# Performance work log

Measured on AMD Instinct MI355X. Metric: run time of the kernel, lower is better.

Reference implementation:

```python
import jax, jax.numpy as jnp
import numpy as np

D_IN = 1024
D_OUT = 1024
NUM_HEADS = 16
HEAD_DIM = D_OUT // NUM_HEADS


def setup_inputs() -> dict:
    key = jax.random.key(0)
    ks = jax.random.split(key, 6)
    s = 0.02
    return {
        "x": jax.random.normal(ks[0], (4, 2048, D_IN), dtype=jnp.float32),
        "W_q": jax.random.normal(ks[1], (D_IN, D_OUT), dtype=jnp.float32) * s,
        "W_k": jax.random.normal(ks[2], (D_IN, D_OUT), dtype=jnp.float32) * s,
        "W_v": jax.random.normal(ks[3], (D_IN, D_OUT), dtype=jnp.float32) * s,
        "W_o": jax.random.normal(ks[4], (D_OUT, D_OUT), dtype=jnp.float32) * s,
        "b_o": jax.random.normal(ks[5], (D_OUT,), dtype=jnp.float32) * s,
    }


def reference(x, W_q, W_k, W_v, W_o, b_o):
    b, n, _ = x.shape
    # project and split heads: [b, h, n, d]
    q = (x @ W_q).reshape(b, n, NUM_HEADS, HEAD_DIM).transpose(0, 2, 1, 3)
    k = (x @ W_k).reshape(b, n, NUM_HEADS, HEAD_DIM).transpose(0, 2, 1, 3)
    v = (x @ W_v).reshape(b, n, NUM_HEADS, HEAD_DIM).transpose(0, 2, 1, 3)
    scores = jnp.einsum("bhqd,bhkd->bhqk", q, k)
    causal = jnp.tril(jnp.ones((n, n), dtype=bool))  # True = keep
    scores = jnp.where(causal, scores, -jnp.inf)
    attn = jax.nn.softmax(scores / np.sqrt(HEAD_DIM).astype(np.float32), axis=-1)
    ctx = jnp.einsum("bhqk,bhkd->bhqd", attn, v)
    ctx = ctx.transpose(0, 2, 1, 3).reshape(b, n, D_OUT)
    return ctx @ W_o + b_o
```

## Files before the change

### kernel.cpp

```cpp
#include <hip/hip_runtime.h>
#include <hip/hip_bf16.h>

#define NHEADS 16
#define HDIM 64
#define SEQ 2048
#define BATCH 4
#define DMODEL 1024
#define MTOT (BATCH * SEQ)

typedef short v8s __attribute__((ext_vector_type(8)));
typedef short v4s __attribute__((ext_vector_type(4)));
typedef float v4f __attribute__((ext_vector_type(4)));
typedef float v16f __attribute__((ext_vector_type(16)));
typedef unsigned int v4u __attribute__((ext_vector_type(4)));
typedef unsigned short u16;
typedef unsigned int u32;

__device__ __forceinline__ u16 f2bf(float f) {
    union { float f; unsigned u; } v; v.f = f;
    unsigned r = v.u + 0x7FFFu + ((v.u >> 16) & 1u);
    return (u16)(r >> 16);
}

__device__ __forceinline__ void g2l16(const u16* g, short* l) {
    __builtin_amdgcn_global_load_lds(
        (const __attribute__((address_space(1))) u32*)g,
        (__attribute__((address_space(3))) u32*)l, 16, 0, 0);
}

__device__ __forceinline__ unsigned pk_bf16(float a, float b) {
    unsigned r;
    asm("v_cvt_pk_bf16_f32 %0, %1, %2" : "=v"(r) : "v"(a), "v"(b));
    return r;
}
__device__ __forceinline__ void pl32swap(unsigned& x, unsigned& y) {
    asm("v_permlane32_swap_b32 %0, %1" : "+v"(x), "+v"(y));
}
__device__ __forceinline__ v8s build_pa(float a0, float a1, float a2, float a3,
                                        float b0, float b1, float b2, float b3) {
    unsigned X  = pk_bf16(a0, a1);
    unsigned X2 = pk_bf16(a2, a3);
    unsigned Y  = pk_bf16(b0, b1);
    unsigned Y2 = pk_bf16(b2, b3);
    pl32swap(X, Y);
    pl32swap(X2, Y2);
    v4u w; w[0] = X; w[1] = X2; w[2] = Y; w[3] = Y2;
    return __builtin_bit_cast(v8s, w);
}

__global__ __launch_bounds__(256)
void xcvt(const float* __restrict__ x, u16* __restrict__ xb)
{
    size_t i = ((size_t)blockIdx.x * 256 + threadIdx.x) * 8;
    v4f a = *(const v4f*)&x[i];
    v4f b = *(const v4f*)&x[i + 4];
    v8s p;
#pragma unroll
    for (int e = 0; e < 4; ++e) p[e] = (short)f2bf(a[e]);
#pragma unroll
    for (int e = 0; e < 4; ++e) p[4 + e] = (short)f2bf(b[e]);
    *(v8s*)&xb[i] = p;
}

__device__ __forceinline__ void transpose_body(
    const float* __restrict__ src, u16* __restrict__ dst, int k0, int n0)
{
    __shared__ __align__(8) short Ts[64 * 68];
    const int t = threadIdx.x;
    const int n4 = (t & 15) * 4, kl = t >> 4;
#pragma unroll
    for (int it = 0; it < 4; ++it) {
        int k = kl + 16 * it;
        v4f v = *(const v4f*)&src[(size_t)(k0 + k) * DMODEL + n0 + n4];
        v4s p;
#pragma unroll
        for (int e = 0; e < 4; ++e) p[e] = (short)f2bf(v[e]);
        *(v4s*)&Ts[k * 68 + n4] = p;
    }
    __syncthreads();
    const int nl = t >> 4, k4 = (t & 15) * 4;
#pragma unroll
    for (int it = 0; it < 4; ++it) {
        int n = nl + 16 * it;
        v4s o;
#pragma unroll
        for (int e = 0; e < 4; ++e) o[e] = Ts[(k4 + e) * 68 + n];
        *(v4s*)&dst[(size_t)(n0 + n) * DMODEL + k0 + k4] = o;
    }
}

__global__ __launch_bounds__(256)
void transpose_w(const float* __restrict__ src, u16* __restrict__ dst)
{
    transpose_body(src, dst, blockIdx.x * 64, blockIdx.y * 64);
}

__global__ __launch_bounds__(256)
void transpose_w4(const float* __restrict__ s0, const float* __restrict__ s1,
                  const float* __restrict__ s2, const float* __restrict__ s3,
                  u16* __restrict__ dst)
{
    const int z = blockIdx.z;
    const float* src = (z == 0) ? s0 : (z == 1) ? s1 : (z == 2) ? s2 : s3;
    transpose_body(src, dst + (size_t)z * DMODEL * DMODEL,
                   blockIdx.x * 64, blockIdx.y * 64);
}

#define QSCALE (0.125f * 1.44269504088896f)

__device__ __forceinline__ void qkv_epilogue(
    v4f (&acc)[4][4], int which, int n0, int m0, int wn, int wm,
    int l15, int quad, u16* Qb, u16* Kb, u16* Vt)
{
    if (which == 2) {
#pragma unroll
        for (int i = 0; i < 4; ++i)
#pragma unroll
            for (int j = 0; j < 4; ++j) {
                int col = n0 + wn + j * 16 + l15;
                int h = col >> 6, d = col & 63;
                int m = m0 + wm + i * 16 + quad * 4;
                int b = m >> 11, n = m & (SEQ - 1);
                v4s pv;
#pragma unroll
                for (int r = 0; r < 4; ++r) pv[r] = (short)f2bf(acc[i][j][r]);
                *(v4s*)&Vt[((size_t)(b * NHEADS + h) * HDIM + d) * SEQ + n] = pv;
            }
    } else {
        u16* Ob = (which == 0) ? Qb : Kb;
        const float scale = (which == 0) ? QSCALE : 1.0f;
#pragma unroll
        for (int i = 0; i < 4; ++i)
#pragma unroll
            for (int j = 0; j < 4; ++j) {
                int col = n0 + wn + j * 16 + l15;
                int h = col >> 6, d = col & 63;
#pragma unroll
                for (int r = 0; r < 4; ++r) {
                    int m = m0 + wm + i * 16 + quad * 4 + r;
                    int b = m >> 11, n = m & (SEQ - 1);
                    Ob[((size_t)(b * NHEADS + h) * SEQ + n) * HDIM + d] =
                        f2bf(acc[i][j][r] * scale);
                }
            }
    }
}

__global__ __launch_bounds__(256, 2)
void qkv_fast(const u16* __restrict__ xb, const u16* __restrict__ Wt,
              u16* __restrict__ Qb, u16* __restrict__ Kb, u16* __restrict__ Vt)
{
    __shared__ __align__(16) short As[128 * 64];
    __shared__ __align__(16) short Bs[128 * 64];

    const int which = blockIdx.z;
    const u16* W = Wt + (size_t)which * DMODEL * DMODEL;

    const int n0 = blockIdx.x * 128;
    const int m0 = blockIdx.y * 128;
    const int t = threadIdx.x;
    const int lane = t & 63;
    const int l15 = lane & 15;
    const int quad = lane >> 4;
    const int wave = t >> 6;
    const int wm = (wave >> 1) * 64;
    const int wn = (wave & 1) * 64;
    const int srow = t >> 3;
    const int sc8 = (t & 7) * 8;

    v4f acc[4][4];
#pragma unroll
    for (int i = 0; i < 4; ++i)
#pragma unroll
        for (int j = 0; j < 4; ++j) acc[i][j] = {0.f, 0.f, 0.f, 0.f};

    for (int k0 = 0; k0 < DMODEL; k0 += 64) {
        __syncthreads();
#pragma unroll
        for (int c = 0; c < 4; ++c) {
            g2l16(&xb[(size_t)(m0 + c * 32 + srow) * DMODEL + k0 + sc8],
                  &As[(c * 32 + srow) * 64 + sc8]);
            g2l16(&W[(size_t)(n0 + c * 32 + srow) * DMODEL + k0 + sc8],
                  &Bs[(c * 32 + srow) * 64 + sc8]);
        }
        __syncthreads();

#pragma unroll
        for (int kh = 0; kh < 2; ++kh) {
            v8s af[4], bf[4];
#pragma unroll
            for (int i = 0; i < 4; ++i)
                af[i] = *(const v8s*)
                    &As[(wm + i * 16 + l15) * 64 + kh * 32 + quad * 8];
#pragma unroll
            for (int j = 0; j < 4; ++j)
                bf[j] = *(const v8s*)
                    &Bs[(wn + j * 16 + l15) * 64 + kh * 32 + quad * 8];
#pragma unroll
            for (int i = 0; i < 4; ++i)
#pragma unroll
                for (int j = 0; j < 4; ++j)
                    acc[i][j] = __builtin_amdgcn_mfma_f32_16x16x32_bf16(
                        af[i], bf[j], acc[i][j], 0, 0, 0);
        }
    }
    qkv_epilogue(acc, which, n0, m0, wn, wm, l15, quad, Qb, Kb, Vt);
}

__global__ __launch_bounds__(256, 2)
void qkv_slow(const float* __restrict__ x, const u16* __restrict__ Wt,
              u16* __restrict__ Qb, u16* __restrict__ Kb, u16* __restrict__ Vt)
{
    __shared__ __align__(16) short As[128 * 32];
    __shared__ __align__(16) short Bs[128 * 32];

    const int which = blockIdx.z;
    const u16* W = Wt + (size_t)which * DMODEL * DMODEL;

    const int n0 = blockIdx.x * 128;
    const int m0 = blockIdx.y * 128;
    const int t = threadIdx.x;
    const int lane = t & 63;
    const int l15 = lane & 15;
    const int quad = lane >> 4;
    const int wave = t >> 6;
    const int wm = (wave >> 1) * 64;
    const int wn = (wave & 1) * 64;
    const int srow = t >> 2;
    const int sc8 = (t & 3) * 8;

    v4f acc[4][4];
#pragma unroll
    for (int i = 0; i < 4; ++i)
#pragma unroll
        for (int j = 0; j < 4; ++j) acc[i][j] = {0.f, 0.f, 0.f, 0.f};

    for (int k0 = 0; k0 < DMODEL; k0 += 32) {
        __syncthreads();
        g2l16(&W[(size_t)(n0 + srow) * DMODEL + k0 + sc8], &Bs[srow * 32 + sc8]);
        g2l16(&W[(size_t)(n0 + 64 + srow) * DMODEL + k0 + sc8],
              &Bs[(64 + srow) * 32 + sc8]);
#pragma unroll
        for (int it = 0; it < 2; ++it) {
            int row = srow + 64 * it;
            const float* xp = &x[(size_t)(m0 + row) * DMODEL + k0 + sc8];
            v4f x0 = *(const v4f*)xp;
            v4f x1 = *(const v4f*)(xp + 4);
            v8s av;
#pragma unroll
            for (int e = 0; e < 4; ++e) av[e] = (short)f2bf(x0[e]);
#pragma unroll
            for (int e = 0; e < 4; ++e) av[4 + e] = (short)f2bf(x1[e]);
            *(v8s*)&As[row * 32 + sc8] = av;
        }
        __syncthreads();

        v8s af[4], bf[4];
#pragma unroll
        for (int i = 0; i < 4; ++i)
            af[i] = *(const v8s*)&As[(wm + i * 16 + l15) * 32 + quad * 8];
#pragma unroll
        for (int j = 0; j < 4; ++j)
            bf[j] = *(const v8s*)&Bs[(wn + j * 16 + l15) * 32 + quad * 8];
#pragma unroll
        for (int i = 0; i < 4; ++i)
#pragma unroll
            for (int j = 0; j < 4; ++j)
                acc[i][j] = __builtin_amdgcn_mfma_f32_16x16x32_bf16(
                    af[i], bf[j], acc[i][j], 0, 0, 0);
    }
    qkv_epilogue(acc, which, n0, m0, wn, wm, l15, quad, Qb, Kb, Vt);
}

#define VXOR(d) ((((d) & 7) << 1) | (((d) >> 3) & 1))

__global__ __launch_bounds__(256, 2)
void attn(const u16* __restrict__ Qb, const u16* __restrict__ Kb,
          const u16* __restrict__ Vt, u16* __restrict__ Cx)
{
    __shared__ __align__(16) short Ks[128 * 64];
    __shared__ __align__(16) short Vs[64 * 128];

    const int ell = blockIdx.x;
    const int xcd = ell & 7;
    const int rest = ell >> 3;
    const int p = rest & 7;
    const int bh = ((rest >> 3) << 3) | xcd;

    const int t = threadIdx.x;
    const int lane = t & 63;
    const int l31 = lane & 31;
    const int hi = lane >> 5;
    const int wave = t >> 6;
    const int koff = hi * 8;

    const u16* Qh = Qb + (size_t)bh * SEQ * HDIM;
    const u16* Kh = Kb + (size_t)bh * SEQ * HDIM;
    const u16* Vh = Vt + (size_t)bh * HDIM * SEQ;

    const int krow = t >> 3;
    const int kslot = t & 7;
    const int vrow = t >> 4;
    const int vslot = t & 15;
    const int b = bh >> 4, h = bh & 15;

#pragma unroll 1
    for (int phase = 0; phase < 2; ++phase) {
        const int qt = phase ? p : (15 - p);
        const int q0w = qt * 128 + wave * 32;

        v8s qf[4];
#pragma unroll
        for (int dc = 0; dc < 4; ++dc)
            qf[dc] = *(const v8s*)
                &Qh[(size_t)(q0w + l31) * HDIM + dc * 16 + koff];

        v16f o0, o1;
#pragma unroll
        for (int r = 0; r < 16; ++r) { o0[r] = 0.f; o1[r] = 0.f; }
        float ls = 0.f;

        v8s pk[4], pv[4];
#pragma unroll
        for (int it = 0; it < 4; ++it)
            pk[it] = *(const v8s*)
                &Kh[(size_t)(it * 32 + krow) * HDIM + kslot * 8];
#pragma unroll
        for (int it = 0; it < 4; ++it)
            pv[it] = *(const v8s*)
                &Vh[(size_t)(it * 16 + vrow) * SEQ + vslot * 8];

#pragma unroll 1
        for (int kb = 0; kb <= qt; ++kb) {
            __syncthreads();
#pragma unroll
            for (int it = 0; it < 4; ++it) {
                int row = it * 32 + krow;
                *(v8s*)&Ks[row * 64 + ((kslot ^ (row & 7)) << 3)] = pk[it];
            }
#pragma unroll
            for (int it = 0; it < 4; ++it) {
                int d = it * 16 + vrow;
                *(v8s*)&Vs[d * 128 + ((vslot ^ VXOR(d)) << 3)] = pv[it];
            }
            __syncthreads();

            if (kb < qt) {
                const int kn = (kb + 1) * 128;
#pragma unroll
                for (int it = 0; it < 4; ++it)
                    pk[it] = *(const v8s*)
                        &Kh[(size_t)(kn + it * 32 + krow) * HDIM + kslot * 8];
#pragma unroll
                for (int it = 0; it < 4; ++it)
                    pv[it] = *(const v8s*)
                        &Vh[(size_t)(it * 16 + vrow) * SEQ + kn + vslot * 8];
            }

#pragma unroll
            for (int k2 = 0; k2 < 2; ++k2) {
                const int kbase = kb * 128 + k2 * 64;
                if (kbase > q0w + 31) continue;
                const bool diag = (kbase + 63 > q0w);
                const int qrow = q0w + l31;

                v16f st0, st1;
#pragma unroll
                for (int r = 0; r < 16; ++r) { st0[r] = 0.f; st1[r] = 0.f; }
#pragma unroll
                for (int dc = 0; dc < 4; ++dc) {
                    const int ds = dc * 2 + hi;
                    const int r0 = k2 * 64 + l31;
                    const int r1 = k2 * 64 + 32 + l31;
                    v8s kf0 = *(const v8s*)
                        &Ks[r0 * 64 + ((ds ^ (r0 & 7)) << 3)];
                    v8s kf1 = *(const v8s*)
                        &Ks[r1 * 64 + ((ds ^ (r1 & 7)) << 3)];
                    st0 = __builtin_amdgcn_mfma_f32_32x32x16_bf16(
                        kf0, qf[dc], st0, 0, 0, 0);
                    st1 = __builtin_amdgcn_mfma_f32_32x32x16_bf16(
                        kf1, qf[dc], st1, 0, 0, 0);
                }

                v16f pe0, pe1;
                if (!diag) {
#pragma unroll
                    for (int r = 0; r < 16; ++r) {
                        pe0[r] = exp2f(st0[r]);
                        pe1[r] = exp2f(st1[r]);
                    }
                } else {
#pragma unroll
                    for (int r = 0; r < 16; ++r) {
                        int kl = kbase + (r & 3) + 8 * (r >> 2) + 4 * hi;
                        pe0[r] = (kl > qrow) ? 0.f : exp2f(st0[r]);
                        pe1[r] = (kl + 32 > qrow) ? 0.f : exp2f(st1[r]);
                    }
                }
#pragma unroll
                for (int r = 0; r < 16; ++r) ls += pe0[r] + pe1[r];

                v8s pa0 = build_pa(pe0[0], pe0[1], pe0[2], pe0[3],
                                   pe0[4], pe0[5], pe0[6], pe0[7]);
                v8s pa1 = build_pa(pe0[8], pe0[9], pe0[10], pe0[11],
                                   pe0[12], pe0[13], pe0[14], pe0[15]);
                v8s pa2 = build_pa(pe1[0], pe1[1], pe1[2], pe1[3],
                                   pe1[4], pe1[5], pe1[6], pe1[7]);
                v8s pa3 = build_pa(pe1[8], pe1[9], pe1[10], pe1[11],
                                   pe1[12], pe1[13], pe1[14], pe1[15]);

#pragma unroll
                for (int kc = 0; kc < 4; ++kc) {
                    v8s pav = (kc == 0) ? pa0 : (kc == 1) ? pa1
                              : (kc == 2) ? pa2 : pa3;
                    const int ks = k2 * 8 + kc * 2 + hi;
                    const int d0 = l31, d1 = 32 + l31;
                    v8s vf0 = *(const v8s*)
                        &Vs[d0 * 128 + ((ks ^ VXOR(d0)) << 3)];
                    v8s vf1 = *(const v8s*)
                        &Vs[d1 * 128 + ((ks ^ VXOR(d1)) << 3)];
                    o0 = __builtin_amdgcn_mfma_f32_32x32x16_bf16(
                        pav, vf0, o0, 0, 0, 0);
                    o1 = __builtin_amdgcn_mfma_f32_32x32x16_bf16(
                        pav, vf1, o1, 0, 0, 0);
                }
            }
        }

        ls += __shfl_xor(ls, 32, 64);
        float inv = 1.f / ls;
#pragma unroll
        for (int r = 0; r < 16; ++r) {
            int m = (r & 3) + 8 * (r >> 2) + 4 * hi;
            float im = __shfl(inv, m, 64);
            size_t idx = ((size_t)(b * SEQ + q0w + m)) * DMODEL
                         + h * HDIM + l31;
            Cx[idx] = f2bf(o0[r] * im);
            Cx[idx + 32] = f2bf(o1[r] * im);
        }
    }
}

__global__ __launch_bounds__(256, 2)
void out_gemm(const u16* __restrict__ Cx, const u16* __restrict__ WoT,
              const float* __restrict__ bo, float* __restrict__ Y)
{
    __shared__ __align__(16) short As[128 * 64];
    __shared__ __align__(16) short Bs[128 * 64];

    const int n0 = blockIdx.x * 128;
    const int m0 = blockIdx.y * 128;
    const int t = threadIdx.x;
    const int lane = t & 63;
    const int l15 = lane & 15;
    const int quad = lane >> 4;
    const int wave = t >> 6;
    const int wm = (wave >> 1) * 64;
    const int wn = (wave & 1) * 64;
    const int srow = t >> 3;
    const int sc8 = (t & 7) * 8;

    v4f acc[4][4];
#pragma unroll
    for (int i = 0; i < 4; ++i)
#pragma unroll
        for (int j = 0; j < 4; ++j) acc[i][j] = {0.f, 0.f, 0.f, 0.f};

    for (int k0 = 0; k0 < DMODEL; k0 += 64) {
        __syncthreads();
#pragma unroll
        for (int c = 0; c < 4; ++c) {
            g2l16(&Cx[(size_t)(m0 + c * 32 + srow) * DMODEL + k0 + sc8],
                  &As[(c * 32 + srow) * 64 + sc8]);
            g2l16(&WoT[(size_t)(n0 + c * 32 + srow) * DMODEL + k0 + sc8],
                  &Bs[(c * 32 + srow) * 64 + sc8]);
        }
        __syncthreads();

#pragma unroll
        for (int kh = 0; kh < 2; ++kh) {
            v8s af[4], bf[4];
#pragma unroll
            for (int i = 0; i < 4; ++i)
                af[i] = *(const v8s*)
                    &As[(wm + i * 16 + l15) * 64 + kh * 32 + quad * 8];
#pragma unroll
            for (int j = 0; j < 4; ++j)
                bf[j] = *(const v8s*)
                    &Bs[(wn + j * 16 + l15) * 64 + kh * 32 + quad * 8];
#pragma unroll
            for (int i = 0; i < 4; ++i)
#pragma unroll
                for (int j = 0; j < 4; ++j)
                    acc[i][j] = __builtin_amdgcn_mfma_f32_16x16x32_bf16(
                        af[i], bf[j], acc[i][j], 0, 0, 0);
        }
    }

#pragma unroll
    for (int i = 0; i < 4; ++i)
#pragma unroll
        for (int j = 0; j < 4; ++j) {
            int col = n0 + wn + j * 16 + l15;
            float bias = bo[col];
#pragma unroll
            for (int r = 0; r < 4; ++r) {
                int m = m0 + wm + i * 16 + quad * 4 + r;
                Y[(size_t)m * DMODEL + col] = acc[i][j][r] + bias;
            }
        }
}

extern "C" void kernel_launch(void* const* d_in, const int* in_sizes, int n_in,
                              void* d_out, int out_size, void* d_ws,
                              size_t ws_size, hipStream_t stream)
{
    const float* x  = (const float*)d_in[0];
    const float* Wq = (const float*)d_in[1];
    const float* Wk = (const float*)d_in[2];
    const float* Wv = (const float*)d_in[3];
    const float* Wo = (const float*)d_in[4];
    const float* bo = (const float*)d_in[5];
    float* Y = (float*)d_out;

    const size_t per = (size_t)BATCH * NHEADS * SEQ * HDIM;
    const size_t wsz = (size_t)DMODEL * DMODEL;
    u16* base = (u16*)d_ws;

    if (ws_size >= (size_t)72 * 1024 * 1024) {
        u16* xb  = base;
        u16* Cx  = base;
        u16* Wt4 = base + per;
        u16* Qb  = base + per + 4 * wsz;
        u16* Kb  = Qb + per;
        u16* Vt  = Kb + per;

        xcvt<<<MTOT * DMODEL / (256 * 8), 256, 0, stream>>>(x, xb);
        transpose_w4<<<dim3(16, 16, 4), 256, 0, stream>>>(Wq, Wk, Wv, Wo, Wt4);
        qkv_fast<<<dim3(DMODEL / 128, MTOT / 128, 3), 256, 0, stream>>>(
            xb, Wt4, Qb, Kb, Vt);
        attn<<<512, 256, 0, stream>>>(Qb, Kb, Vt, Cx);
        out_gemm<<<dim3(DMODEL / 128, MTOT / 128), 256, 0, stream>>>(
            Cx, Wt4 + 3 * wsz, bo, Y);
    } else {
        u16* Wt  = base;
        u16* Cx  = base;
        u16* Qb  = base + per;
        u16* WoT = base + per;
        u16* Kb  = base + 2 * per;
        u16* Vt  = base + 3 * per;

        transpose_w<<<dim3(16, 16), 256, 0, stream>>>(Wq, Wt);
        transpose_w<<<dim3(16, 16), 256, 0, stream>>>(Wk, Wt + wsz);
        transpose_w<<<dim3(16, 16), 256, 0, stream>>>(Wv, Wt + 2 * wsz);
        qkv_slow<<<dim3(DMODEL / 128, MTOT / 128, 3), 256, 0, stream>>>(
            x, Wt, Qb, Kb, Vt);
        attn<<<512, 256, 0, stream>>>(Qb, Kb, Vt, Cx);
        transpose_w<<<dim3(16, 16), 256, 0, stream>>>(Wo, WoT);
        out_gemm<<<dim3(DMODEL / 128, MTOT / 128), 256, 0, stream>>>(
            Cx, WoT, bo, Y);
    }
}
```

Baseline: 261.0 us.

## Merge prep kernels, swap MFMA operands for vectorized Q/K stores, raise occupancy

The x bf16 conversion and the four weight transposes now run in a single prep launch, removing one kernel launch and its tail. For the Q and K projections the MFMA operands are swapped, so each lane holds four consecutive head-dim values and writes one 8-byte vector store instead of four scattered 2-byte stores. The launch bound on qkv_fast goes from 2 to 3 blocks per CU, which may constrain registers and cause spills.

```diff
diff --git a/kernel.cpp b/kernel.cpp
--- a/kernel.cpp
+++ b/kernel.cpp
@@ -48,20 +48,6 @@
     return __builtin_bit_cast(v8s, w);
 }
 
-__global__ __launch_bounds__(256)
-void xcvt(const float* __restrict__ x, u16* __restrict__ xb)
-{
-    size_t i = ((size_t)blockIdx.x * 256 + threadIdx.x) * 8;
-    v4f a = *(const v4f*)&x[i];
-    v4f b = *(const v4f*)&x[i + 4];
-    v8s p;
-#pragma unroll
-    for (int e = 0; e < 4; ++e) p[e] = (short)f2bf(a[e]);
-#pragma unroll
-    for (int e = 0; e < 4; ++e) p[4 + e] = (short)f2bf(b[e]);
-    *(v8s*)&xb[i] = p;
-}
-
 __device__ __forceinline__ void transpose_body(
     const float* __restrict__ src, u16* __restrict__ dst, int k0, int n0)
 {
@@ -96,14 +82,29 @@
 }
 
 __global__ __launch_bounds__(256)
-void transpose_w4(const float* __restrict__ s0, const float* __restrict__ s1,
-                  const float* __restrict__ s2, const float* __restrict__ s3,
-                  u16* __restrict__ dst)
-{
-    const int z = blockIdx.z;
-    const float* src = (z == 0) ? s0 : (z == 1) ? s1 : (z == 2) ? s2 : s3;
-    transpose_body(src, dst + (size_t)z * DMODEL * DMODEL,
-                   blockIdx.x * 64, blockIdx.y * 64);
+void prep(const float* __restrict__ x, u16* __restrict__ xb,
+          const float* __restrict__ s0, const float* __restrict__ s1,
+          const float* __restrict__ s2, const float* __restrict__ s3,
+          u16* __restrict__ wdst)
+{
+    const int blk = blockIdx.x;
+    if (blk < 1024) {
+        const int z = blk >> 8;
+        const int rem = blk & 255;
+        const float* src = (z == 0) ? s0 : (z == 1) ? s1 : (z == 2) ? s2 : s3;
+        transpose_body(src, wdst + (size_t)z * DMODEL * DMODEL,
+                       (rem & 15) * 64, (rem >> 4) * 64);
+    } else {
+        size_t i = ((size_t)(blk - 1024) * 256 + threadIdx.x) * 8;
+        v4f a = *(const v4f*)&x[i];
+        v4f b = *(const v4f*)&x[i + 4];
+        v8s p;
+#pragma unroll
+        for (int e = 0; e < 4; ++e) p[e] = (short)f2bf(a[e]);
+#pragma unroll
+        for (int e = 0; e < 4; ++e) p[4 + e] = (short)f2bf(b[e]);
+        *(v8s*)&xb[i] = p;
+    }
 }
 
 #define QSCALE (0.125f * 1.44269504088896f)
@@ -146,7 +147,58 @@
     }
 }
 
-__global__ __launch_bounds__(256, 2)
+template <bool SWAP>
+__device__ __forceinline__ void qkv_loop(
+    const u16* __restrict__ xb, const u16* __restrict__ W,
+    int m0, int n0, int t, short* As, short* Bs, v4f (&acc)[4][4])
+{
+    const int lane = t & 63;
+    const int l15 = lane & 15;
+    const int quad = lane >> 4;
+    const int wave = t >> 6;
+    const int wm = (wave >> 1) * 64;
+    const int wn = (wave & 1) * 64;
+    const int srow = t >> 3;
+    const int sc8 = (t & 7) * 8;
+
+    for (int k0 = 0; k0 < DMODEL; k0 += 64) {
+        __syncthreads();
+#pragma unroll
+        for (int c = 0; c < 4; ++c) {
+            g2l16(&xb[(size_t)(m0 + c * 32 + srow) * DMODEL + k0 + sc8],
+                  &As[(c * 32 + srow) * 64 + sc8]);
+            g2l16(&W[(size_t)(n0 + c * 32 + srow) * DMODEL + k0 + sc8],
+                  &Bs[(c * 32 + srow) * 64 + sc8]);
+        }
+        __syncthreads();
+
+#pragma unroll
+        for (int kh = 0; kh < 2; ++kh) {
+            v8s af[4], bf[4];
+#pragma unroll
+            for (int i = 0; i < 4; ++i)
+                af[i] = *(const v8s*)
+                    &As[(wm + i * 16 + l15) * 64 + kh * 32 + quad * 8];
+#pragma unroll
+            for (int j = 0; j < 4; ++j)
+                bf[j] = *(const v8s*)
+                    &Bs[(wn + j * 16 + l15) * 64 + kh * 32 + quad * 8];
+#pragma unroll
+            for (int i = 0; i < 4; ++i)
+#pragma unroll
+                for (int j = 0; j < 4; ++j) {
+                    if (SWAP)
+                        acc[i][j] = __builtin_amdgcn_mfma_f32_16x16x32_bf16(
+                            bf[j], af[i], acc[i][j], 0, 0, 0);
+                    else
+                        acc[i][j] = __builtin_amdgcn_mfma_f32_16x16x32_bf16(
+                            af[i], bf[j], acc[i][j], 0, 0, 0);
+                }
+        }
+    }
+}
+
+__global__ __launch_bounds__(256, 3)
 void qkv_fast(const u16* __restrict__ xb, const u16* __restrict__ Wt,
               u16* __restrict__ Qb, u16* __restrict__ Kb, u16* __restrict__ Vt)
 {
@@ -165,8 +217,6 @@
     const int wave = t >> 6;
     const int wm = (wave >> 1) * 64;
     const int wn = (wave & 1) * 64;
-    const int srow = t >> 3;
-    const int sc8 = (t & 7) * 8;
 
     v4f acc[4][4];
 #pragma unroll
@@ -174,37 +224,42 @@
 #pragma unroll
         for (int j = 0; j < 4; ++j) acc[i][j] = {0.f, 0.f, 0.f, 0.f};
 
-    for (int k0 = 0; k0 < DMODEL; k0 += 64) {
-        __syncthreads();
-#pragma unroll
-        for (int c = 0; c < 4; ++c) {
-            g2l16(&xb[(size_t)(m0 + c * 32 + srow) * DMODEL + k0 + sc8],
-                  &As[(c * 32 + srow) * 64 + sc8]);
-            g2l16(&W[(size_t)(n0 + c * 32 + srow) * DMODEL + k0 + sc8],
-                  &Bs[(c * 32 + srow) * 64 + sc8]);
-        }
-        __syncthreads();
-
-#pragma unroll
-        for (int kh = 0; kh < 2; ++kh) {
-            v8s af[4], bf[4];
-#pragma unroll
-            for (int i = 0; i < 4; ++i)
-                af[i] = *(const v8s*)
-                    &As[(wm + i * 16 + l15) * 64 + kh * 32 + quad * 8];
-#pragma unroll
-            for (int j = 0; j < 4; ++j)
-                bf[j] = *(const v8s*)
-                    &Bs[(wn + j * 16 + l15) * 64 + kh * 32 + quad * 8];
-#pragma unroll
-            for (int i = 0; i < 4; ++i)
-#pragma unroll
-                for (int j = 0; j < 4; ++j)
-                    acc[i][j] = __builtin_amdgcn_mfma_f32_16x16x32_bf16(
-                        af[i], bf[j], acc[i][j], 0, 0, 0);
-        }
-    }
-    qkv_epilogue(acc, which, n0, m0, wn, wm, l15, quad, Qb, Kb, Vt);
+    if (which == 2) {
+        qkv_loop<false>(xb, W, m0, n0, t, As, Bs, acc);
+#pragma unroll
+        for (int i = 0; i < 4; ++i)
+#pragma unroll
+            for (int j = 0; j < 4; ++j) {
+                int col = n0 + wn + j * 16 + l15;
+                int h = col >> 6, d = col & 63;
+                int m = m0 + wm + i * 16 + quad * 4;
+                int b = m >> 11, n = m & (SEQ - 1);
+                v4s pv;
+#pragma unroll
+                for (int r = 0; r < 4; ++r) pv[r] = (short)f2bf(acc[i][j][r]);
+                *(v4s*)&Vt[((size_t)(b * NHEADS + h) * HDIM + d) * SEQ + n] = pv;
+            }
+    } else {
+        qkv_loop<true>(xb, W, m0, n0, t, As, Bs, acc);
+        u16* Ob = which ? Kb : Qb;
+        const float scale = which ? 1.0f : QSCALE;
+#pragma unroll
+        for (int i = 0; i < 4; ++i) {
+            int m = m0 + wm + i * 16 + l15;
+            int b = m >> 11, n = m & (SEQ - 1);
+#pragma unroll
+            for (int j = 0; j < 4; ++j) {
+                int colb = n0 + wn + j * 16 + quad * 4;
+                int h = colb >> 6, d0 = colb & 63;
+                v4s pv;
+#pragma unroll
+                for (int r = 0; r < 4; ++r)
+                    pv[r] = (short)f2bf(acc[i][j][r] * scale);
+                *(v4s*)&Ob[((size_t)(b * NHEADS + h) * SEQ + n) * HDIM + d0]
+                    = pv;
+            }
+        }
+    }
 }
 
 __global__ __launch_bounds__(256, 2)
@@ -535,8 +590,8 @@
         u16* Kb  = Qb + per;
         u16* Vt  = Kb + per;
 
-        xcvt<<<MTOT * DMODEL / (256 * 8), 256, 0, stream>>>(x, xb);
-        transpose_w4<<<dim3(16, 16, 4), 256, 0, stream>>>(Wq, Wk, Wv, Wo, Wt4);
+        prep<<<1024 + MTOT * DMODEL / (256 * 8), 256, 0, stream>>>(
+            x, xb, Wq, Wk, Wv, Wo, Wt4);
         qkv_fast<<<dim3(DMODEL / 128, MTOT / 128, 3), 256, 0, stream>>>(
             xb, Wt4, Qb, Kb, Vt);
         attn<<<512, 256, 0, stream>>>(Qb, Kb, Vt, Cx);
```

Measured after the change: 262.4 us. About the same (+0.5%).
